# Optimization experiments

Hardware: AMD Instinct MI355X
Metric: run time of the kernel (lower is better)

## Reference

```python
import jax, jax.numpy as jnp
import numpy as np

TEMPERATURE = 0.07
ALPHA = 1.0
GAMMA = 2.0
EPS = 1e-12  # F.normalize eps


def _l2_normalize(x):
    # matches F.normalize: x / max(||x||_2, eps)
    norm = jnp.sqrt(jnp.sum(x * x, axis=-1, keepdims=True))
    return x / jnp.maximum(norm, EPS)


def setup_inputs() -> dict:
    key = jax.random.key(0)
    k1, k2 = jax.random.split(key)
    B, D = 8192, 64
    image_features = jax.random.normal(k1, (B, D), dtype=jnp.float32)
    text_features = jax.random.normal(k2, (B, D), dtype=jnp.float32)
    return {"image_features": image_features, "text_features": text_features}


def reference(image_features, text_features):
    img = _l2_normalize(image_features)
    txt = _l2_normalize(text_features)
    logits = jnp.einsum("bd,cd->bc", img, txt) / TEMPERATURE  # [B, B]
    B = logits.shape[0]
    idx = jnp.arange(B)

    logp_row = jax.nn.log_softmax(logits, axis=-1)  # i2t CE source
    logp_col = jax.nn.log_softmax(logits, axis=0)   # t2i CE source

    diag_logp_row = logp_row[idx, idx]
    diag_logp_col = logp_col[idx, idx]

    # focal weight uses ROW-softmax positive prob for BOTH directions (as in source)
    p_pos = jnp.exp(diag_logp_row)
    w = ALPHA * (1.0 - p_pos) ** GAMMA

    focal_i2t = jnp.mean(w * (-diag_logp_row))
    focal_t2i = jnp.mean(w * (-diag_logp_col))
    return (focal_i2t + focal_t2i) / 2.0
```

## Files before the change

kernel.cpp:

```cpp
#include <hip/hip_runtime.h>
#include <hip/hip_bf16.h>


#define NB 8192
#define ND 64

constexpr float INV_T = 1.0f / 0.07f;
constexpr float LOG2E = 1.4426950408889634f;
constexpr float LN2   = 0.6931471805599453f;
constexpr float K1    = INV_T * LOG2E;

typedef float  floatx4 __attribute__((ext_vector_type(4)));
typedef short  bf16x8  __attribute__((ext_vector_type(8)));

__global__ __launch_bounds__(256)
void norm_kernel(const float* __restrict__ img, const float* __restrict__ txt,
                 __hip_bfloat16* __restrict__ imgB,
                 __hip_bfloat16* __restrict__ txtB,
                 float* __restrict__ diag)
{
    const int lane = threadIdx.x & 63;
    const int row  = blockIdx.x * 4 + (threadIdx.x >> 6);
    float x = img[row * ND + lane];
    float t = txt[row * ND + lane];
    float sx = x * x, st = t * t;
    #pragma unroll
    for (int o = 1; o < 64; o <<= 1) {
        sx += __shfl_xor(sx, o, 64);
        st += __shfl_xor(st, o, 64);
    }
    const float nx = x / fmaxf(sqrtf(sx), 1e-12f);
    const float nt = t / fmaxf(sqrtf(st), 1e-12f);
    float pd = nx * nt;
    #pragma unroll
    for (int o = 1; o < 64; o <<= 1) pd += __shfl_xor(pd, o, 64);
    imgB[row * ND + lane] = __float2bfloat16(nx);
    txtB[row * ND + lane] = __float2bfloat16(nt);
    if (lane == 0) diag[row] = pd * INV_T;
}

__global__ __launch_bounds__(256)
void score_kernel(const __hip_bfloat16* __restrict__ imgB,
                  const __hip_bfloat16* __restrict__ txtB,
                  float* __restrict__ rowPart,
                  float* __restrict__ colPart)
{
    const int wid   = threadIdx.x >> 6;
    const int lane  = threadIdx.x & 63;
    const int gw    = blockIdx.x * 4 + wid;
    const int strip = gw >> 5;
    const int chunk = gw & 31;
    const int m = lane & 15;
    const int q = lane >> 4;

    const bf16x8* __restrict__ A = (const bf16x8*)imgB;
    const bf16x8* __restrict__ B = (const bf16x8*)txtB;

    const int rowbase = strip * 64;
    bf16x8 a[4][2];
    #pragma unroll
    for (int it = 0; it < 4; ++it) {
        const int r = rowbase + it * 16 + m;
        a[it][0] = A[r * 8 + q];
        a[it][1] = A[r * 8 + 4 + q];
    }

    float rs[16];
    #pragma unroll
    for (int i = 0; i < 16; ++i) rs[i] = 0.f;

    for (int t = 0; t < 16; ++t) {
        const int n = chunk * 256 + t * 16 + m;
        const bf16x8 b0 = B[n * 8 + q];
        const bf16x8 b1 = B[n * 8 + 4 + q];
        floatx4 acc[4];
        #pragma unroll
        for (int it = 0; it < 4; ++it) {
            floatx4 z = {0.f, 0.f, 0.f, 0.f};
            z = __builtin_amdgcn_mfma_f32_16x16x32_bf16(a[it][0], b0, z, 0, 0, 0);
            acc[it] = __builtin_amdgcn_mfma_f32_16x16x32_bf16(a[it][1], b1, z, 0, 0, 0);
        }
        float cs = 0.f;
        #pragma unroll
        for (int it = 0; it < 4; ++it) {
            #pragma unroll
            for (int r = 0; r < 4; ++r) {
                const float e = __builtin_amdgcn_exp2f((acc[it][r] - 1.0f) * K1);
                rs[it * 4 + r] += e;
                cs += e;
            }
        }
        cs += __shfl_xor(cs, 16, 64);
        cs += __shfl_xor(cs, 32, 64);
        if (q == 0) colPart[strip * NB + n] = cs;
    }

    #pragma unroll
    for (int idx = 0; idx < 16; ++idx) {
        float v = rs[idx];
        v += __shfl_xor(v, 1, 64);
        v += __shfl_xor(v, 2, 64);
        v += __shfl_xor(v, 4, 64);
        v += __shfl_xor(v, 8, 64);
        if (m == idx) {
            const int it = idx >> 2, r = idx & 3;
            rowPart[chunk * NB + rowbase + it * 16 + q * 4 + r] = v;
        }
    }
}

__global__ __launch_bounds__(256)
void finish_kernel(const float* __restrict__ rowPart,
                   const float* __restrict__ colPart,
                   const float* __restrict__ diag,
                   float* __restrict__ out)
{
    const int i = blockIdx.x * 256 + threadIdx.x;
    float rowS = 0.f, colS = 0.f;
    #pragma unroll 4
    for (int c = 0; c < 32; ++c)  rowS += rowPart[c * NB + i];
    #pragma unroll 4
    for (int s = 0; s < 128; ++s) colS += colPart[s * NB + i];
    const float d     = diag[i];
    const float lse_r = INV_T + __builtin_amdgcn_logf(rowS) * LN2;
    const float lse_c = INV_T + __builtin_amdgcn_logf(colS) * LN2;
    const float lpr = d - lse_r;
    const float lpc = d - lse_c;
    const float p   = __builtin_amdgcn_exp2f(lpr * LOG2E);
    const float om  = 1.f - p;
    float contrib = om * om * (-lpr - lpc) * (0.5f / (float)NB);

    #pragma unroll
    for (int o = 1; o < 64; o <<= 1) contrib += __shfl_xor(contrib, o, 64);
    __shared__ float red[4];
    if ((threadIdx.x & 63) == 0) red[threadIdx.x >> 6] = contrib;
    __syncthreads();
    if (threadIdx.x == 0)
        atomicAdd(out, red[0] + red[1] + red[2] + red[3]);
}

extern "C" void kernel_launch(void* const* d_in, const int* in_sizes, int n_in,
                              void* d_out, int out_size, void* d_ws, size_t ws_size,
                              hipStream_t stream)
{
    const float* img = (const float*)d_in[0];
    const float* txt = (const float*)d_in[1];

    char* ws = (char*)d_ws;
    __hip_bfloat16* imgB = (__hip_bfloat16*)(ws);
    __hip_bfloat16* txtB = (__hip_bfloat16*)(ws + (1u << 20));
    float* diag    = (float*)(ws + (2u << 20));
    float* rowPart = (float*)(ws + (2u << 20) + (1u << 16));
    float* colPart = (float*)(ws + (3u << 20) + (1u << 16));

    hipMemsetAsync(d_out, 0, sizeof(float), stream);

    norm_kernel<<<NB / 4, 256, 0, stream>>>(img, txt, imgB, txtB, diag);
    score_kernel<<<1024, 256, 0, stream>>>(imgB, txtB, rowPart, colPart);
    finish_kernel<<<NB / 256, 256, 0, stream>>>(rowPart, colPart, diag, (float*)d_out);
}
```

Before: 101.6 us.

## Prefetch B fragments, fuse exp with FMA, merge diag reduction, drop memset

The score kernel now software-pipelines the text-fragment loads, fetching the next tile's B operands while computing on the current one. The exp argument becomes a single FMA, and column sums are built as a pairwise tree. The norm kernel computes the diagonal dot product in the same shuffle reduction as the norms instead of a second reduction pass. It also zeroes the output itself, which removes the separate hipMemsetAsync launch. The prefetch raises register pressure, and the unnormalized-dot diagonal differs slightly in rounding.

```diff
diff --git a/kernel.cpp b/kernel.cpp
--- a/kernel.cpp
+++ b/kernel.cpp
@@ -17,26 +17,26 @@
 void norm_kernel(const float* __restrict__ img, const float* __restrict__ txt,
                  __hip_bfloat16* __restrict__ imgB,
                  __hip_bfloat16* __restrict__ txtB,
-                 float* __restrict__ diag)
+                 float* __restrict__ diag,
+                 float* __restrict__ out)
 {
+    if (blockIdx.x == 0 && threadIdx.x == 0) out[0] = 0.f;
     const int lane = threadIdx.x & 63;
     const int row  = blockIdx.x * 4 + (threadIdx.x >> 6);
-    float x = img[row * ND + lane];
-    float t = txt[row * ND + lane];
-    float sx = x * x, st = t * t;
+    const float x = img[row * ND + lane];
+    const float t = txt[row * ND + lane];
+    float sx = x * x, st = t * t, sxt = x * t;
     #pragma unroll
     for (int o = 1; o < 64; o <<= 1) {
-        sx += __shfl_xor(sx, o, 64);
-        st += __shfl_xor(st, o, 64);
+        sx  += __shfl_xor(sx,  o, 64);
+        st  += __shfl_xor(st,  o, 64);
+        sxt += __shfl_xor(sxt, o, 64);
     }
-    const float nx = x / fmaxf(sqrtf(sx), 1e-12f);
-    const float nt = t / fmaxf(sqrtf(st), 1e-12f);
-    float pd = nx * nt;
-    #pragma unroll
-    for (int o = 1; o < 64; o <<= 1) pd += __shfl_xor(pd, o, 64);
-    imgB[row * ND + lane] = __float2bfloat16(nx);
-    txtB[row * ND + lane] = __float2bfloat16(nt);
-    if (lane == 0) diag[row] = pd * INV_T;
+    const float nx_den = fmaxf(sqrtf(sx), 1e-12f);
+    const float nt_den = fmaxf(sqrtf(st), 1e-12f);
+    imgB[row * ND + lane] = __float2bfloat16(x / nx_den);
+    txtB[row * ND + lane] = __float2bfloat16(t / nt_den);
+    if (lane == 0) diag[row] = sxt / (nx_den * nt_den) * INV_T;
 }
 
 __global__ __launch_bounds__(256)
@@ -53,8 +53,8 @@
     const int m = lane & 15;
     const int q = lane >> 4;
 
-    const bf16x8* __restrict__ A = (const bf16x8*)imgB;
-    const bf16x8* __restrict__ B = (const bf16x8*)txtB;
+    const bf16x8* __restrict__ A  = (const bf16x8*)imgB;
+    const bf16x8* __restrict__ Bp = (const bf16x8*)txtB;
 
     const int rowbase = strip * 64;
     bf16x8 a[4][2];
@@ -65,34 +65,42 @@
         a[it][1] = A[r * 8 + 4 + q];
     }
 
+    const int colbase = chunk * 256 + m;
+    bf16x8 b0 = Bp[colbase * 8 + q];
+    bf16x8 b1 = Bp[colbase * 8 + 4 + q];
+
     float rs[16];
     #pragma unroll
     for (int i = 0; i < 16; ++i) rs[i] = 0.f;
 
+    const floatx4 ZERO = {0.f, 0.f, 0.f, 0.f};
+
+    #pragma unroll 2
     for (int t = 0; t < 16; ++t) {
-        const int n = chunk * 256 + t * 16 + m;
-        const bf16x8 b0 = B[n * 8 + q];
-        const bf16x8 b1 = B[n * 8 + 4 + q];
-        floatx4 acc[4];
+        const int nn = colbase + (((t + 1) & 15) << 4);
+        const bf16x8 pb0 = Bp[nn * 8 + q];
+        const bf16x8 pb1 = Bp[nn * 8 + 4 + q];
+
+        float csp[4];
         #pragma unroll
         for (int it = 0; it < 4; ++it) {
-            floatx4 z = {0.f, 0.f, 0.f, 0.f};
-            z = __builtin_amdgcn_mfma_f32_16x16x32_bf16(a[it][0], b0, z, 0, 0, 0);
-            acc[it] = __builtin_amdgcn_mfma_f32_16x16x32_bf16(a[it][1], b1, z, 0, 0, 0);
+            floatx4 z = __builtin_amdgcn_mfma_f32_16x16x32_bf16(a[it][0], b0, ZERO, 0, 0, 0);
+            floatx4 acc = __builtin_amdgcn_mfma_f32_16x16x32_bf16(a[it][1], b1, z, 0, 0, 0);
+            const float e0 = __builtin_amdgcn_exp2f(__builtin_fmaf(acc[0], K1, -K1));
+            const float e1 = __builtin_amdgcn_exp2f(__builtin_fmaf(acc[1], K1, -K1));
+            const float e2 = __builtin_amdgcn_exp2f(__builtin_fmaf(acc[2], K1, -K1));
+            const float e3 = __builtin_amdgcn_exp2f(__builtin_fmaf(acc[3], K1, -K1));
+            rs[it * 4 + 0] += e0;
+            rs[it * 4 + 1] += e1;
+            rs[it * 4 + 2] += e2;
+            rs[it * 4 + 3] += e3;
+            csp[it] = (e0 + e1) + (e2 + e3);
         }
-        float cs = 0.f;
-        #pragma unroll
-        for (int it = 0; it < 4; ++it) {
-            #pragma unroll
-            for (int r = 0; r < 4; ++r) {
-                const float e = __builtin_amdgcn_exp2f((acc[it][r] - 1.0f) * K1);
-                rs[it * 4 + r] += e;
-                cs += e;
-            }
-        }
+        float cs = (csp[0] + csp[1]) + (csp[2] + csp[3]);
         cs += __shfl_xor(cs, 16, 64);
         cs += __shfl_xor(cs, 32, 64);
-        if (q == 0) colPart[strip * NB + n] = cs;
+        if (q == 0) colPart[strip * NB + colbase + (t << 4)] = cs;
+        b0 = pb0; b1 = pb1;
     }
 
     #pragma unroll
@@ -153,9 +161,7 @@
     float* rowPart = (float*)(ws + (2u << 20) + (1u << 16));
     float* colPart = (float*)(ws + (3u << 20) + (1u << 16));
 
-    hipMemsetAsync(d_out, 0, sizeof(float), stream);
-
-    norm_kernel<<<NB / 4, 256, 0, stream>>>(img, txt, imgB, txtB, diag);
+    norm_kernel<<<NB / 4, 256, 0, stream>>>(img, txt, imgB, txtB, diag, (float*)d_out);
     score_kernel<<<1024, 256, 0, stream>>>(imgB, txtB, rowPart, colPart);
     finish_kernel<<<NB / 256, 256, 0, stream>>>(rowPart, colPart, diag, (float*)d_out);
 }
```

Measured after the change: 98.57 us. 3.0% less time.
